# Kernel tuning notes

Hardware: AMD Instinct MI355X
Metric: run time of the kernel (lower is better)

## Reference

```python
import jax, jax.numpy as jnp
import numpy as np

B, N, C, H, W = 32, 8, 256, 4, 4


def setup_inputs() -> dict:
    key = jax.random.key(0)
    k1, k2 = jax.random.split(key)
    pred = jax.random.normal(k1, (B, N, C, H, W), dtype=jnp.float32)
    gt = jax.random.normal(k2, (B, N, C, H, W), dtype=jnp.float32)
    return {"pred": pred, "gt": gt}


def reference(pred, gt):
    b, n, c, h, w = pred.shape
    M = b * n * h * w
    # (B,N,C,H,W) -> (B,N,H,W,C) -> (M, C)
    p = jnp.transpose(pred, (0, 1, 3, 4, 2)).reshape(M, c)
    # (B,N,C,H,W) -> (C,B,N,H,W) -> (C, M)
    g = jnp.transpose(gt, (2, 0, 1, 3, 4)).reshape(c, M)
    lossmat = p @ g  # (M, M) similarity matrix
    # CrossEntropy with target = arange(M): -mean(log_softmax diag)
    logp = jax.nn.log_softmax(lossmat, axis=1)
    loss = -jnp.mean(jnp.diagonal(logp))
    # accuracy (no grad in original)
    top1 = jnp.argmax(lossmat, axis=1)
    acc = jnp.mean((top1 == jnp.arange(M)).astype(jnp.float32)) * 100.0
    return (loss, acc)
```

## Files before the change

kernel.cpp:

```cpp
#include <hip/hip_runtime.h>
#include <cstdint>

typedef __bf16 bf16x8 __attribute__((ext_vector_type(8)));
typedef float floatx4 __attribute__((ext_vector_type(4)));


#define OFF_X     (0u)
#define OFF_Y     (2u*1024*1024)
#define OFF_PMAX  (4u*1024*1024)
#define OFF_PSUM  (5u*1024*1024)
#define OFF_DIAG  (6u*1024*1024)

#define AS1C(p) ((const __attribute__((address_space(1))) void*)(const void*)(p))
#define AS3(p)  ((__attribute__((address_space(3))) void*)(void*)(p))

__global__ __launch_bounds__(256) void transpose_stage(
    const float* __restrict__ pred, const float* __restrict__ gt,
    unsigned short* __restrict__ Xs, unsigned short* __restrict__ Ys,
    float* __restrict__ out) {
  int blk = blockIdx.x;
  if (blk == 0 && threadIdx.x == 0) { out[0] = 0.f; out[1] = 0.f; }
  const float* src;
  unsigned short* dst;
  int slab;
  if (blk < 256) { src = pred; dst = Xs; slab = blk; }
  else           { src = gt;   dst = Ys; slab = blk - 256; }
  const float* sb = src + slab * 4096;
  const int rb = slab >> 3, rowhi = slab & 7;
  const int t = threadIdx.x;
  #pragma unroll
  for (int half = 0; half < 2; ++half) {
    int c_ = half * 256 + t;
    int rowlo = c_ & 15;
    int quad  = (c_ >> 4) & 3;
    int kk    = (c_ >> 6) & 1;
    int s     = c_ >> 7;
    int k0 = s * 64 + kk * 32 + quad * 8;
    unsigned int packed[4];
    #pragma unroll
    for (int jj = 0; jj < 4; ++jj) {
      unsigned int lohi[2];
      #pragma unroll
      for (int e = 0; e < 2; ++e) {
        float f = sb[(k0 + jj * 2 + e) * 16 + rowlo];
        unsigned int u = __float_as_uint(f);
        lohi[e] = (u + 0x7FFFu + ((u >> 16) & 1u)) >> 16;
      }
      packed[jj] = lohi[0] | (lohi[1] << 16);
    }
    unsigned short* o = dst + rb * 32768 +
        (unsigned)(s * 1024 + kk * 512 + rowhi * 64 + quad * 16 + rowlo) * 8;
    uint4 v; v.x = packed[0]; v.y = packed[1]; v.z = packed[2]; v.w = packed[3];
    *reinterpret_cast<uint4*>(o) = v;
  }
}

__global__ __launch_bounds__(256) void gemm_softmax_partial(
    const unsigned short* __restrict__ Xs, const unsigned short* __restrict__ Ys,
    float* __restrict__ pmax, float* __restrict__ psum, float* __restrict__ diag) {
  __shared__ __align__(16) unsigned short As[8192];
  __shared__ __align__(16) unsigned short Bs[8192];
  const int t = threadIdx.x;
  const int wave = t >> 6, lane = t & 63;
  const int rg = wave >> 1, cg = wave & 1;
  const int bR = blockIdx.x, bC = blockIdx.y;
  const unsigned short* Ag = Xs + bR * 32768;
  const unsigned short* Bg = Ys + bC * 32768;

  floatx4 acc[4][4];
  const floatx4 zero = {0.f, 0.f, 0.f, 0.f};
  #pragma unroll
  for (int i = 0; i < 4; ++i)
    #pragma unroll
    for (int j = 0; j < 4; ++j) acc[i][j] = zero;

  for (int s = 0; s < 4; ++s) {
    #pragma unroll
    for (int it = 0; it < 4; ++it) {
      int chunk = it * 256 + t;
      __builtin_amdgcn_global_load_lds(AS1C(Ag + s * 8192 + chunk * 8),
                                       AS3(As + chunk * 8), 16, 0, 0);
      __builtin_amdgcn_global_load_lds(AS1C(Bg + s * 8192 + chunk * 8),
                                       AS3(Bs + chunk * 8), 16, 0, 0);
    }
    __syncthreads();
    #pragma unroll
    for (int kk = 0; kk < 2; ++kk) {
      bf16x8 a[4], b[4];
      #pragma unroll
      for (int fr = 0; fr < 4; ++fr)
        a[fr] = *reinterpret_cast<const bf16x8*>(
            As + (unsigned)(kk * 512 + (rg * 4 + fr) * 64 + lane) * 8);
      #pragma unroll
      for (int fc = 0; fc < 4; ++fc)
        b[fc] = *reinterpret_cast<const bf16x8*>(
            Bs + (unsigned)(kk * 512 + (cg * 4 + fc) * 64 + lane) * 8);
      #pragma unroll
      for (int fr = 0; fr < 4; ++fr)
        #pragma unroll
        for (int fc = 0; fc < 4; ++fc)
          acc[fr][fc] = __builtin_amdgcn_mfma_f32_16x16x32_bf16(
              a[fr], b[fc], acc[fr][fc], 0, 0, 0);
    }
    if (s < 3) __syncthreads();
  }

  const int quad = lane >> 4, lc = lane & 15;

  if (bR == bC && rg == cg) {
    #pragma unroll
    for (int fr = 0; fr < 4; ++fr)
      #pragma unroll
      for (int r = 0; r < 4; ++r)
        if (lc == quad * 4 + r)
          diag[bR * 128 + rg * 64 + fr * 16 + lc] = acc[fr][fr][r];
  }

  const int g = bC * 2 + cg;
  #pragma unroll
  for (int fr = 0; fr < 4; ++fr) {
    #pragma unroll
    for (int r = 0; r < 4; ++r) {
      float v0 = acc[fr][0][r], v1 = acc[fr][1][r];
      float v2 = acc[fr][2][r], v3 = acc[fr][3][r];
      float m = fmaxf(fmaxf(v0, v1), fmaxf(v2, v3));
      #pragma unroll
      for (int sh = 1; sh < 16; sh <<= 1) m = fmaxf(m, __shfl_xor(m, sh, 64));
      float ss = __expf(v0 - m) + __expf(v1 - m) +
                 __expf(v2 - m) + __expf(v3 - m);
      #pragma unroll
      for (int sh = 1; sh < 16; sh <<= 1) ss += __shfl_xor(ss, sh, 64);
      if (lc == 0) {
        int grow = bR * 128 + rg * 64 + fr * 16 + quad * 4 + r;
        int p = g * 4096 + grow;
        pmax[p] = m; psum[p] = ss;
      }
    }
  }
}

__global__ __launch_bounds__(64) void combine_rows(
    const float* __restrict__ pmax, const float* __restrict__ psum,
    const float* __restrict__ diag, float* __restrict__ out) {
  int row = blockIdx.x * 64 + threadIdx.x;
  float M = -3.4e38f;
  #pragma unroll 8
  for (int b = 0; b < 64; ++b) M = fmaxf(M, pmax[b * 4096 + row]);
  float S = 0.f;
  #pragma unroll 8
  for (int b = 0; b < 64; ++b)
    S += psum[b * 4096 + row] * __expf(pmax[b * 4096 + row] - M);
  float d = diag[row];
  float lossr = logf(S) + M - d;
  float corr = (d == M) ? 1.f : 0.f;
  #pragma unroll
  for (int sh = 1; sh < 64; sh <<= 1) {
    lossr += __shfl_xor(lossr, sh, 64);
    corr  += __shfl_xor(corr,  sh, 64);
  }
  if (threadIdx.x == 0) {
    atomicAdd(out + 0, lossr * (1.f / 4096.f));
    atomicAdd(out + 1, corr * (100.f / 4096.f));
  }
}

extern "C" void kernel_launch(void* const* d_in, const int* in_sizes, int n_in,
                              void* d_out, int out_size, void* d_ws, size_t ws_size,
                              hipStream_t stream) {
  const float* pred = (const float*)d_in[0];
  const float* gt   = (const float*)d_in[1];
  char* w = (char*)d_ws;
  unsigned short* Xbf = (unsigned short*)(w + OFF_X);
  unsigned short* Ybf = (unsigned short*)(w + OFF_Y);
  float* pmax  = (float*)(w + OFF_PMAX);
  float* psum  = (float*)(w + OFF_PSUM);
  float* diag  = (float*)(w + OFF_DIAG);
  float* out   = (float*)d_out;

  transpose_stage<<<512, 256, 0, stream>>>(pred, gt, Xbf, Ybf, out);
  dim3 g1(32, 32);
  gemm_softmax_partial<<<g1, 256, 0, stream>>>(Xbf, Ybf, pmax, psum, diag);
  combine_rows<<<64, 64, 0, stream>>>(pmax, psum, diag, out);
}
```

Baseline: 98.46 us.

## Fuse transpose, GEMM-softmax and row combine into one persistent kernel with grid barriers

Replaces the three kernel launches with a single persistent kernel of 512 blocks. Atomic-counter grid barriers separate the transpose, GEMM-plus-partial-softmax and row-combine phases, and each block handles two GEMM tiles. The partial max/sum arrays are moved to a row-major layout so one wave can combine a row with a single coalesced load. This removes launch gaps and the under-parallelised 64-block combine, but it relies on all 512 blocks being co-resident, adds a memset launch and spin-wait overhead, and halves the GEMM grid parallelism per pass.

New measurement: 283.2 us. 2.88x slower.

```diff
diff --git a/kernel.cpp b/kernel.cpp
--- a/kernel.cpp
+++ b/kernel.cpp
@@ -10,157 +10,174 @@
 #define OFF_PMAX  (4u*1024*1024)
 #define OFF_PSUM  (5u*1024*1024)
 #define OFF_DIAG  (6u*1024*1024)
+#define OFF_CTR   (6u*1024*1024 + 65536u)
 
 #define AS1C(p) ((const __attribute__((address_space(1))) void*)(const void*)(p))
 #define AS3(p)  ((__attribute__((address_space(3))) void*)(void*)(p))
 
-__global__ __launch_bounds__(256) void transpose_stage(
+__device__ __forceinline__ void grid_barrier(unsigned* ctr, unsigned nblk) {
+  __threadfence();
+  __syncthreads();
+  if (threadIdx.x == 0) {
+    atomicAdd(ctr, 1u);
+    while (atomicAdd(ctr, 0u) < nblk) __builtin_amdgcn_s_sleep(2);
+  }
+  __syncthreads();
+  __threadfence();
+}
+
+__global__ __launch_bounds__(256, 2) void dpc_fused(
     const float* __restrict__ pred, const float* __restrict__ gt,
     unsigned short* __restrict__ Xs, unsigned short* __restrict__ Ys,
+    float* __restrict__ pmax, float* __restrict__ psum,
+    float* __restrict__ diag, unsigned* __restrict__ ctr,
     float* __restrict__ out) {
-  int blk = blockIdx.x;
-  if (blk == 0 && threadIdx.x == 0) { out[0] = 0.f; out[1] = 0.f; }
-  const float* src;
-  unsigned short* dst;
-  int slab;
-  if (blk < 256) { src = pred; dst = Xs; slab = blk; }
-  else           { src = gt;   dst = Ys; slab = blk - 256; }
-  const float* sb = src + slab * 4096;
-  const int rb = slab >> 3, rowhi = slab & 7;
-  const int t = threadIdx.x;
-  #pragma unroll
-  for (int half = 0; half < 2; ++half) {
-    int c_ = half * 256 + t;
-    int rowlo = c_ & 15;
-    int quad  = (c_ >> 4) & 3;
-    int kk    = (c_ >> 6) & 1;
-    int s     = c_ >> 7;
-    int k0 = s * 64 + kk * 32 + quad * 8;
-    unsigned int packed[4];
-    #pragma unroll
-    for (int jj = 0; jj < 4; ++jj) {
-      unsigned int lohi[2];
-      #pragma unroll
-      for (int e = 0; e < 2; ++e) {
-        float f = sb[(k0 + jj * 2 + e) * 16 + rowlo];
-        unsigned int u = __float_as_uint(f);
-        lohi[e] = (u + 0x7FFFu + ((u >> 16) & 1u)) >> 16;
-      }
-      packed[jj] = lohi[0] | (lohi[1] << 16);
-    }
-    unsigned short* o = dst + rb * 32768 +
-        (unsigned)(s * 1024 + kk * 512 + rowhi * 64 + quad * 16 + rowlo) * 8;
-    uint4 v; v.x = packed[0]; v.y = packed[1]; v.z = packed[2]; v.w = packed[3];
-    *reinterpret_cast<uint4*>(o) = v;
-  }
-}
-
-__global__ __launch_bounds__(256) void gemm_softmax_partial(
-    const unsigned short* __restrict__ Xs, const unsigned short* __restrict__ Ys,
-    float* __restrict__ pmax, float* __restrict__ psum, float* __restrict__ diag) {
   __shared__ __align__(16) unsigned short As[8192];
   __shared__ __align__(16) unsigned short Bs[8192];
+  __shared__ float redl[4], redc[4];
+  const int blk = blockIdx.x;
   const int t = threadIdx.x;
   const int wave = t >> 6, lane = t & 63;
-  const int rg = wave >> 1, cg = wave & 1;
-  const int bR = blockIdx.x, bC = blockIdx.y;
-  const unsigned short* Ag = Xs + bR * 32768;
-  const unsigned short* Bg = Ys + bC * 32768;
-
-  floatx4 acc[4][4];
-  const floatx4 zero = {0.f, 0.f, 0.f, 0.f};
-  #pragma unroll
-  for (int i = 0; i < 4; ++i)
-    #pragma unroll
-    for (int j = 0; j < 4; ++j) acc[i][j] = zero;
-
-  for (int s = 0; s < 4; ++s) {
-    #pragma unroll
-    for (int it = 0; it < 4; ++it) {
-      int chunk = it * 256 + t;
-      __builtin_amdgcn_global_load_lds(AS1C(Ag + s * 8192 + chunk * 8),
-                                       AS3(As + chunk * 8), 16, 0, 0);
-      __builtin_amdgcn_global_load_lds(AS1C(Bg + s * 8192 + chunk * 8),
-                                       AS3(Bs + chunk * 8), 16, 0, 0);
-    }
+
+  {
+    if (blk == 0 && t == 0) { out[0] = 0.f; out[1] = 0.f; }
+    const float* src;
+    unsigned short* dst;
+    int slab;
+    if (blk < 256) { src = pred; dst = Xs; slab = blk; }
+    else           { src = gt;   dst = Ys; slab = blk - 256; }
+    const float* sb = src + slab * 4096;
+    const int rb = slab >> 3, rowhi = slab & 7;
+    #pragma unroll
+    for (int half = 0; half < 2; ++half) {
+      int c_ = half * 256 + t;
+      int rowlo = c_ & 15;
+      int quad  = (c_ >> 4) & 3;
+      int kk    = (c_ >> 6) & 1;
+      int s     = c_ >> 7;
+      int k0 = s * 64 + kk * 32 + quad * 8;
+      unsigned int packed[4];
+      #pragma unroll
+      for (int jj = 0; jj < 4; ++jj) {
+        unsigned int lohi[2];
+        #pragma unroll
+        for (int e = 0; e < 2; ++e) {
+          float f = sb[(k0 + jj * 2 + e) * 16 + rowlo];
+          unsigned int u = __float_as_uint(f);
+          lohi[e] = (u + 0x7FFFu + ((u >> 16) & 1u)) >> 16;
+        }
+        packed[jj] = lohi[0] | (lohi[1] << 16);
+      }
+      unsigned short* o = dst + rb * 32768 +
+          (unsigned)(s * 1024 + kk * 512 + rowhi * 64 + quad * 16 + rowlo) * 8;
+      uint4 v; v.x = packed[0]; v.y = packed[1]; v.z = packed[2]; v.w = packed[3];
+      *reinterpret_cast<uint4*>(o) = v;
+    }
+  }
+  grid_barrier(ctr + 0, 512);
+
+  const int rg = wave >> 1, cg_ = wave & 1;
+  const int quad = lane >> 4, lc = lane & 15;
+  for (int tile = blk; tile < 1024; tile += 512) {
+    const int bR = tile >> 5, bC = tile & 31;
+    const unsigned short* Ag = Xs + bR * 32768;
+    const unsigned short* Bg = Ys + bC * 32768;
+
+    floatx4 acc[4][4];
+    const floatx4 zero = {0.f, 0.f, 0.f, 0.f};
+    #pragma unroll
+    for (int i = 0; i < 4; ++i)
+      #pragma unroll
+      for (int j = 0; j < 4; ++j) acc[i][j] = zero;
+
     __syncthreads();
-    #pragma unroll
-    for (int kk = 0; kk < 2; ++kk) {
-      bf16x8 a[4], b[4];
+    for (int s = 0; s < 4; ++s) {
+      #pragma unroll
+      for (int it = 0; it < 4; ++it) {
+        int chunk = it * 256 + t;
+        __builtin_amdgcn_global_load_lds(AS1C(Ag + s * 8192 + chunk * 8),
+                                         AS3(As + chunk * 8), 16, 0, 0);
+        __builtin_amdgcn_global_load_lds(AS1C(Bg + s * 8192 + chunk * 8),
+                                         AS3(Bs + chunk * 8), 16, 0, 0);
+      }
+      __syncthreads();
+      #pragma unroll
+      for (int kk = 0; kk < 2; ++kk) {
+        bf16x8 a[4], b[4];
+        #pragma unroll
+        for (int fr = 0; fr < 4; ++fr)
+          a[fr] = *reinterpret_cast<const bf16x8*>(
+              As + (unsigned)(kk * 512 + (rg * 4 + fr) * 64 + lane) * 8);
+        #pragma unroll
+        for (int fc = 0; fc < 4; ++fc)
+          b[fc] = *reinterpret_cast<const bf16x8*>(
+              Bs + (unsigned)(kk * 512 + (cg_ * 4 + fc) * 64 + lane) * 8);
+        #pragma unroll
+        for (int fr = 0; fr < 4; ++fr)
+          #pragma unroll
+          for (int fc = 0; fc < 4; ++fc)
+            acc[fr][fc] = __builtin_amdgcn_mfma_f32_16x16x32_bf16(
+                a[fr], b[fc], acc[fr][fc], 0, 0, 0);
+      }
+      if (s < 3) __syncthreads();
+    }
+
+    if (bR == bC && rg == cg_) {
       #pragma unroll
       for (int fr = 0; fr < 4; ++fr)
-        a[fr] = *reinterpret_cast<const bf16x8*>(
-            As + (unsigned)(kk * 512 + (rg * 4 + fr) * 64 + lane) * 8);
-      #pragma unroll
-      for (int fc = 0; fc < 4; ++fc)
-        b[fc] = *reinterpret_cast<const bf16x8*>(
-            Bs + (unsigned)(kk * 512 + (cg * 4 + fc) * 64 + lane) * 8);
-      #pragma unroll
-      for (int fr = 0; fr < 4; ++fr)
-        #pragma unroll
-        for (int fc = 0; fc < 4; ++fc)
-          acc[fr][fc] = __builtin_amdgcn_mfma_f32_16x16x32_bf16(
-              a[fr], b[fc], acc[fr][fc], 0, 0, 0);
-    }
-    if (s < 3) __syncthreads();
-  }
-
-  const int quad = lane >> 4, lc = lane & 15;
-
-  if (bR == bC && rg == cg) {
-    #pragma unroll
-    for (int fr = 0; fr < 4; ++fr)
-      #pragma unroll
-      for (int r = 0; r < 4; ++r)
-        if (lc == quad * 4 + r)
-          diag[bR * 128 + rg * 64 + fr * 16 + lc] = acc[fr][fr][r];
-  }
-
-  const int g = bC * 2 + cg;
-  #pragma unroll
-  for (int fr = 0; fr < 4; ++fr) {
-    #pragma unroll
-    for (int r = 0; r < 4; ++r) {
-      float v0 = acc[fr][0][r], v1 = acc[fr][1][r];
-      float v2 = acc[fr][2][r], v3 = acc[fr][3][r];
-      float m = fmaxf(fmaxf(v0, v1), fmaxf(v2, v3));
-      #pragma unroll
-      for (int sh = 1; sh < 16; sh <<= 1) m = fmaxf(m, __shfl_xor(m, sh, 64));
-      float ss = __expf(v0 - m) + __expf(v1 - m) +
-                 __expf(v2 - m) + __expf(v3 - m);
-      #pragma unroll
-      for (int sh = 1; sh < 16; sh <<= 1) ss += __shfl_xor(ss, sh, 64);
-      if (lc == 0) {
-        int grow = bR * 128 + rg * 64 + fr * 16 + quad * 4 + r;
-        int p = g * 4096 + grow;
-        pmax[p] = m; psum[p] = ss;
-      }
-    }
-  }
-}
-
-__global__ __launch_bounds__(64) void combine_rows(
-    const float* __restrict__ pmax, const float* __restrict__ psum,
-    const float* __restrict__ diag, float* __restrict__ out) {
-  int row = blockIdx.x * 64 + threadIdx.x;
-  float M = -3.4e38f;
-  #pragma unroll 8
-  for (int b = 0; b < 64; ++b) M = fmaxf(M, pmax[b * 4096 + row]);
-  float S = 0.f;
-  #pragma unroll 8
-  for (int b = 0; b < 64; ++b)
-    S += psum[b * 4096 + row] * __expf(pmax[b * 4096 + row] - M);
-  float d = diag[row];
-  float lossr = logf(S) + M - d;
-  float corr = (d == M) ? 1.f : 0.f;
-  #pragma unroll
-  for (int sh = 1; sh < 64; sh <<= 1) {
-    lossr += __shfl_xor(lossr, sh, 64);
-    corr  += __shfl_xor(corr,  sh, 64);
-  }
-  if (threadIdx.x == 0) {
-    atomicAdd(out + 0, lossr * (1.f / 4096.f));
-    atomicAdd(out + 1, corr * (100.f / 4096.f));
+        #pragma unroll
+        for (int r = 0; r < 4; ++r)
+          if (lc == quad * 4 + r)
+            diag[bR * 128 + rg * 64 + fr * 16 + lc] = acc[fr][fr][r];
+    }
+
+    const int g = bC * 2 + cg_;
+    #pragma unroll
+    for (int fr = 0; fr < 4; ++fr) {
+      #pragma unroll
+      for (int r = 0; r < 4; ++r) {
+        float v0 = acc[fr][0][r], v1 = acc[fr][1][r];
+        float v2 = acc[fr][2][r], v3 = acc[fr][3][r];
+        float m = fmaxf(fmaxf(v0, v1), fmaxf(v2, v3));
+        #pragma unroll
+        for (int sh = 1; sh < 16; sh <<= 1) m = fmaxf(m, __shfl_xor(m, sh, 64));
+        float ss = __expf(v0 - m) + __expf(v1 - m) +
+                   __expf(v2 - m) + __expf(v3 - m);
+        #pragma unroll
+        for (int sh = 1; sh < 16; sh <<= 1) ss += __shfl_xor(ss, sh, 64);
+        if (lc == 0) {
+          int grow = bR * 128 + rg * 64 + fr * 16 + quad * 4 + r;
+          pmax[grow * 64 + g] = m;
+          psum[grow * 64 + g] = ss;
+        }
+      }
+    }
+  }
+  grid_barrier(ctr + 1, 512);
+
+  {
+    float lacc = 0.f, cacc = 0.f;
+    #pragma unroll
+    for (int r = 0; r < 2; ++r) {
+      int row = blk * 8 + wave * 2 + r;
+      float pm = pmax[row * 64 + lane];
+      float ps = psum[row * 64 + lane];
+      float M = pm;
+      #pragma unroll
+      for (int sh = 1; sh < 64; sh <<= 1) M = fmaxf(M, __shfl_xor(M, sh, 64));
+      float S = ps * __expf(pm - M);
+      #pragma unroll
+      for (int sh = 1; sh < 64; sh <<= 1) S += __shfl_xor(S, sh, 64);
+      float d = diag[row];
+      lacc += logf(S) + M - d;
+      cacc += (d == M) ? 1.f : 0.f;
+    }
+    if (lane == 0) { redl[wave] = lacc; redc[wave] = cacc; }
+    __syncthreads();
+    if (t == 0) {
+      atomicAdd(out + 0, (redl[0] + redl[1] + redl[2] + redl[3]) * (1.f / 4096.f));
+      atomicAdd(out + 1, (redc[0] + redc[1] + redc[2] + redc[3]) * (100.f / 4096.f));
+    }
   }
 }
 
@@ -170,15 +187,15 @@
   const float* pred = (const float*)d_in[0];
   const float* gt   = (const float*)d_in[1];
   char* w = (char*)d_ws;
-  unsigned short* Xbf = (unsigned short*)(w + OFF_X);
-  unsigned short* Ybf = (unsigned short*)(w + OFF_Y);
+  unsigned short* Xs = (unsigned short*)(w + OFF_X);
+  unsigned short* Ys = (unsigned short*)(w + OFF_Y);
   float* pmax  = (float*)(w + OFF_PMAX);
   float* psum  = (float*)(w + OFF_PSUM);
   float* diag  = (float*)(w + OFF_DIAG);
+  unsigned* ctr = (unsigned*)(w + OFF_CTR);
   float* out   = (float*)d_out;
 
-  transpose_stage<<<512, 256, 0, stream>>>(pred, gt, Xbf, Ybf, out);
-  dim3 g1(32, 32);
-  gemm_softmax_partial<<<g1, 256, 0, stream>>>(Xbf, Ybf, pmax, psum, diag);
-  combine_rows<<<64, 64, 0, stream>>>(pmax, psum, diag, out);
+  hipMemsetAsync(ctr, 0, 2 * sizeof(unsigned), stream);
+  dpc_fused<<<512, 256, 0, stream>>>(pred, gt, Xs, Ys, pmax, psum, diag,
+                                     ctr, out);
 }
```
